# Performance work log

Measured on AMD Instinct MI355X. Metric: run time of the kernel, lower is better.

Reference implementation:

```python
import jax, jax.numpy as jnp
import numpy as np

N, E, D, ED, G = 50000, 800000, 64, 32, 50


def setup_inputs() -> dict:
    key = jax.random.key(0)
    ks = jax.random.split(key, 24)
    s = 0.05
    inp = {
        "x": jax.random.normal(ks[0], (N, D), jnp.float32),
        "edge_attr": jax.random.normal(ks[1], (E, ED), jnp.float32),
        "edge_index": jax.random.randint(ks[2], (2, E), 0, N, jnp.int64),
    }
    i = 3
    for step in range(2):
        inp[f"fe{step}_W1"] = jax.random.normal(ks[i], (2 * D + ED, D), jnp.float32) * s; i += 1
        inp[f"fe{step}_b1"] = jnp.zeros((D,), jnp.float32)
        inp[f"fe{step}_W2"] = jax.random.normal(ks[i], (D, D), jnp.float32) * s; i += 1
        inp[f"fe{step}_b2"] = jnp.zeros((D,), jnp.float32)
        inp[f"lstm{step}_Wih"] = jax.random.normal(ks[i], (D, 4 * D), jnp.float32) * s; i += 1
        inp[f"lstm{step}_Whh"] = jax.random.normal(ks[i], (D, 4 * D), jnp.float32) * s; i += 1
        inp[f"lstm{step}_bih"] = jnp.zeros((4 * D,), jnp.float32)
        inp[f"lstm{step}_bhh"] = jnp.zeros((4 * D,), jnp.float32)
    inp["gm_W"] = jax.random.normal(ks[i], (D, G), jnp.float32) * s; i += 1
    inp["gm_b"] = jnp.zeros((G,), jnp.float32)
    inp["fm_W"] = jax.random.normal(ks[i], (D, G), jnp.float32) * s; i += 1
    inp["fm_b"] = jnp.zeros((G,), jnp.float32)
    return inp


def _mpn(x, edge_attr, src, dst, W1, b1, W2, b2):
    # x_i = x[dst] (target), x_j = x[src] (source); aggregate 'add' at dst
    m = jnp.concatenate([x[dst], x[src], edge_attr], axis=1)  # [E, 2D+ED]
    m = jax.nn.relu(m @ W1 + b1) @ W2 + b2                    # [E, D]
    return jax.ops.segment_sum(m, dst, num_segments=x.shape[0])


def _lstm_cell(inp, h, c, Wih, Whh, bih, bhh):
    gates = inp @ Wih + h @ Whh + (bih + bhh)  # [N, 4D], gate order i,f,g,o
    i, f, g, o = jnp.split(gates, 4, axis=1)
    c = jax.nn.sigmoid(f) * c + jax.nn.sigmoid(i) * jnp.tanh(g)
    h = jax.nn.sigmoid(o) * jnp.tanh(c)
    return h, c


def reference(x, edge_attr, edge_index,
              fe0_W1, fe0_b1, fe0_W2, fe0_b2,
              lstm0_Wih, lstm0_Whh, lstm0_bih, lstm0_bhh,
              fe1_W1, fe1_b1, fe1_W2, fe1_b2,
              lstm1_Wih, lstm1_Whh, lstm1_bih, lstm1_bhh,
              gm_W, gm_b, fm_W, fm_b):
    src, dst = edge_index[0], edge_index[1]
    c = jnp.zeros_like(x)
    fes = [(fe0_W1, fe0_b1, fe0_W2, fe0_b2), (fe1_W1, fe1_b1, fe1_W2, fe1_b2)]
    lstms = [(lstm0_Wih, lstm0_Whh, lstm0_bih, lstm0_bhh),
             (lstm1_Wih, lstm1_Whh, lstm1_bih, lstm1_bhh)]
    for step in range(2):
        a = _mpn(x, edge_attr, src, dst, *fes[step])
        # LSTMCell(input=x, (h=a, c=c)) as in the original forward
        x, c = _lstm_cell(x, a, c, *lstms[step])
    g = jax.nn.sigmoid(x @ gm_W + gm_b)   # [N, G]
    h_v_G = x @ fm_W + fm_b               # [N, G]
    return jnp.sum(g * h_v_G, axis=0)     # [G]
```

## Files before the change

### kernel.cpp

```cpp
#include <hip/hip_runtime.h>
#include <hip/hip_bf16.h>

using short8 = __attribute__((ext_vector_type(8))) short;
using f32x4  = __attribute__((ext_vector_type(4))) float;

#define KLP 136

__device__ __forceinline__ unsigned short f2bf(float f) {
  unsigned u = __float_as_uint(f);
  u += 0x7FFFu + ((u >> 16) & 1u);
  return (unsigned short)(u >> 16);
}
__device__ __forceinline__ unsigned pack2(float a, float b) {
  return (unsigned)f2bf(a) | ((unsigned)f2bf(b) << 16);
}
#if __has_builtin(__builtin_amdgcn_rcpf)
__device__ __forceinline__ float fast_rcp(float x) { return __builtin_amdgcn_rcpf(x); }
#else
__device__ __forceinline__ float fast_rcp(float x) { return 1.f / x; }
#endif
__device__ __forceinline__ float sigm(float x) { return fast_rcp(1.f + __expf(-x)); }
__device__ __forceinline__ float tanh_f(float x) { return fmaf(2.f, sigm(2.f * x), -1.f); }

__global__ __launch_bounds__(256) void prep_simple(
    const float* __restrict__ W1_0, const float* __restrict__ Wih0,
    const float* __restrict__ bih0, const float* __restrict__ bhh0,
    const float* __restrict__ W1_1, const float* __restrict__ Wih1,
    const float* __restrict__ bih1, const float* __restrict__ bhh1,
    const float* __restrict__ gmW, const float* __restrict__ fmW,
    unsigned short* __restrict__ W1T,
    unsigned short* __restrict__ WcT,
    float* __restrict__ bG,
    unsigned short* __restrict__ WrT)
{
  int t = blockIdx.x * 256 + threadIdx.x;
  const int per = 10240 + 16384 + 256;
  if (t >= 2 * per + 8192) return;
  if (t >= 2 * per) {
    int r2 = t - 2 * per;
    int o = r2 >> 6, k = r2 & 63;
    float v = 0.f;
    if (o < 50) v = gmW[k * 50 + o];
    else if (o >= 64 && o < 114) v = fmW[k * 50 + (o - 64)];
    WrT[o * 64 + k] = f2bf(v);
    return;
  }
  int step = t / per, r = t % per;
  const float* W1  = step ? W1_1 : W1_0;
  const float* Wih = step ? Wih1 : Wih0;
  const float* bih = step ? bih1 : bih0;
  const float* bhh = step ? bhh1 : bhh0;
  if (r < 10240) {
    int o = r / 160, k = r % 160;
    W1T[step * 10240 + o * 160 + k] = f2bf(W1[k * 64 + o]);
  } else if (r < 26624) {
    int rr = r - 10240;
    int g = rr >> 6, k = rr & 63;
    WcT[step * 32768 + g * 128 + k] = f2bf(Wih[k * 256 + g]);
  } else {
    int g = r - 26624;
    bG[step * 256 + g] = bih[g] + bhh[g];
  }
}

__global__ __launch_bounds__(256) void prep_merge(
    const float* __restrict__ W2_0, const float* __restrict__ Whh0, const float* __restrict__ b2_0,
    const float* __restrict__ W2_1, const float* __restrict__ Whh1, const float* __restrict__ b2_1,
    unsigned short* __restrict__ WcT,
    float* __restrict__ b2h)
{
  int t = blockIdx.x * 256 + threadIdx.x;
  if (t < 32768) {
    int step = t >> 14, r = t & 16383;
    int g = r >> 6, k = r & 63;
    const float* W2  = step ? W2_1 : W2_0;
    const float* Whh = step ? Whh1 : Whh0;
    float v = 0.f;
    for (int j = 0; j < 64; ++j) v = fmaf(W2[k * 64 + j], Whh[j * 256 + g], v);
    WcT[step * 32768 + g * 128 + 64 + k] = f2bf(v);
  } else if (t < 33280) {
    int r = t - 32768;
    int step = r >> 8, g = r & 255;
    const float* b2  = step ? b2_1 : b2_0;
    const float* Whh = step ? Whh1 : Whh0;
    float v = 0.f;
    for (int j = 0; j < 64; ++j) v = fmaf(b2[j], Whh[j * 256 + g], v);
    b2h[step * 256 + g] = v;
  }
}

__global__ __launch_bounds__(256) void convert_x(
    const float* __restrict__ x, unsigned short* __restrict__ xb, int n)
{
  int i = blockIdx.x * 256 + threadIdx.x;
  if (i < n) xb[i] = f2bf(x[i]);
}

__global__ __launch_bounds__(256) void hist_kernel(
    const int* __restrict__ dstI, int* __restrict__ hist, int E)
{
  int e = blockIdx.x * 256 + threadIdx.x;
  if (e < E) atomicAdd(&hist[dstI[e]], 1);
}

__global__ __launch_bounds__(256) void scan_part(
    const int* __restrict__ hist, int2* __restrict__ blockTot, int N)
{
  __shared__ int sD[256], sS[256];
  int t = threadIdx.x;
  int n = blockIdx.x * 256 + t;
  int d = (n < N) ? hist[n] : 0;
  int sg = (d + 15) >> 4;
  sD[t] = d; sS[t] = sg;
  __syncthreads();
  #pragma unroll
  for (int off = 128; off; off >>= 1) {
    if (t < off) { sD[t] += sD[t + off]; sS[t] += sS[t + off]; }
    __syncthreads();
  }
  if (t == 0) blockTot[blockIdx.x] = make_int2(sD[0], sS[0]);
}

__global__ __launch_bounds__(256) void scan_mid(
    const int2* __restrict__ blockTot, int2* __restrict__ blockBase,
    int* __restrict__ nSegTot, int nb)
{
  __shared__ int sD[256], sS[256];
  int t = threadIdx.x;
  int d = 0, s = 0;
  if (t < nb) { int2 v = blockTot[t]; d = v.x; s = v.y; }
  sD[t] = d; sS[t] = s;
  __syncthreads();
  #pragma unroll
  for (int off = 1; off < 256; off <<= 1) {
    int vd = (t >= off) ? sD[t - off] : 0;
    int vs = (t >= off) ? sS[t - off] : 0;
    __syncthreads();
    sD[t] += vd; sS[t] += vs;
    __syncthreads();
  }
  if (t < nb) blockBase[t] = make_int2(sD[t] - d, sS[t] - s);
  if (t == nb - 1) *nSegTot = sS[t];
}

__global__ __launch_bounds__(256) void scan_final(
    const int* __restrict__ hist, const int2* __restrict__ blockBase,
    int* __restrict__ cursor, int4* __restrict__ segInfo, int N)
{
  __shared__ int sD[256], sS[256];
  int t = threadIdx.x;
  int n = blockIdx.x * 256 + t;
  int d = (n < N) ? hist[n] : 0;
  int sg = (d + 15) >> 4;
  sD[t] = d; sS[t] = sg;
  __syncthreads();
  #pragma unroll
  for (int off = 1; off < 256; off <<= 1) {
    int vd = (t >= off) ? sD[t - off] : 0;
    int vs = (t >= off) ? sS[t - off] : 0;
    __syncthreads();
    sD[t] += vd; sS[t] += vs;
    __syncthreads();
  }
  if (n < N) {
    int2 bb = blockBase[blockIdx.x];
    int degBase = bb.x + sD[t] - d;
    int segBase = bb.y + sS[t] - sg;
    cursor[n] = degBase;
    for (int j = 0; j < sg; ++j)
      segInfo[segBase + j] = make_int4(degBase + j * 16, n, min(d - j * 16, 16), 0);
  }
}

__global__ __launch_bounds__(256) void perm_build(
    const int* __restrict__ srcI, const int* __restrict__ dstI,
    int* __restrict__ cursor, int* __restrict__ ePerm,
    int* __restrict__ srcS, int E)
{
  int e = blockIdx.x * 256 + threadIdx.x;
  if (e >= E) return;
  int d = dstI[e];
  int p = atomicAdd(&cursor[d], 1);
  ePerm[p] = e;
  srcS[p] = srcI[e];
}

__global__ __launch_bounds__(256) void edge_gemm_reg(
    const unsigned short* __restrict__ xb,
    const float* __restrict__ ea,
    const int* __restrict__ ePerm,
    const int* __restrict__ srcS,
    const int4* __restrict__ segInfo,
    const int* __restrict__ nSegPtr,
    const unsigned short* __restrict__ W1T,
    const float* __restrict__ b1,
    float* __restrict__ aggrH)
{
  const int t = threadIdx.x;
  const int w = t >> 6, l = t & 63;
  const int quad = l >> 4, lr = l & 15;

  short8 bF[5][4];
  #pragma unroll
  for (int kc = 0; kc < 5; ++kc)
    #pragma unroll
    for (int n = 0; n < 4; ++n)
      bF[kc][n] = *(const short8*)(W1T + (n * 16 + lr) * 160 + kc * 32 + quad * 8);
  float bb[4];
  #pragma unroll
  for (int n = 0; n < 4; ++n) bb[n] = b1[n * 16 + lr];

  const int nSeg = *nSegPtr;
  const int W = gridDim.x * 4;
  int s = blockIdx.x * 4 + w;
  if (s >= nSeg) return;
  int4 si = segInfo[s];
  {
    int pos0 = si.x + min(lr, si.z - 1);
  }
  int pos = si.x + min(lr, si.z - 1);
  int src = srcS[pos];
  int ep  = ePerm[pos];

  while (true) {
    const int sn = s + W;
    const bool more = sn < nSeg;
    int4 si_n = si;
    if (more) si_n = segInfo[sn];

    const int node = si.y, cnt = si.z;

    const short8* pd = (const short8*)(xb + (long long)node * 64);
    const short8* ps = (const short8*)(xb + (long long)src * 64);
    const float4* pe = (const float4*)(ea + (long long)ep * 32 + quad * 8);
    short8 a0 = pd[quad];
    short8 a1 = pd[4 + quad];
    short8 a2 = ps[quad];
    short8 a3 = ps[4 + quad];
    float4 e0 = pe[0];
    float4 e1 = pe[1];

    int src_n = src, ep_n = ep;
    if (more) {
      int pos_n = si_n.x + min(lr, si_n.z - 1);
      src_n = srcS[pos_n];
      ep_n  = ePerm[pos_n];
    }

    union { uint4 u; short8 s8; } cv;
    cv.u = make_uint4(pack2(e0.x, e0.y), pack2(e0.z, e0.w),
                      pack2(e1.x, e1.y), pack2(e1.z, e1.w));
    short8 a4 = cv.s8;

    f32x4 acc[4] = {};
    #pragma unroll
    for (int n = 0; n < 4; ++n) acc[n] = __builtin_amdgcn_mfma_f32_16x16x32_bf16(a0, bF[0][n], acc[n], 0, 0, 0);
    #pragma unroll
    for (int n = 0; n < 4; ++n) acc[n] = __builtin_amdgcn_mfma_f32_16x16x32_bf16(a1, bF[1][n], acc[n], 0, 0, 0);
    #pragma unroll
    for (int n = 0; n < 4; ++n) acc[n] = __builtin_amdgcn_mfma_f32_16x16x32_bf16(a2, bF[2][n], acc[n], 0, 0, 0);
    #pragma unroll
    for (int n = 0; n < 4; ++n) acc[n] = __builtin_amdgcn_mfma_f32_16x16x32_bf16(a3, bF[3][n], acc[n], 0, 0, 0);
    #pragma unroll
    for (int n = 0; n < 4; ++n) acc[n] = __builtin_amdgcn_mfma_f32_16x16x32_bf16(a4, bF[4][n], acc[n], 0, 0, 0);

    #pragma unroll
    for (int n = 0; n < 4; ++n) {
      float sum = 0.f;
      #pragma unroll
      for (int rr = 0; rr < 4; ++rr) {
        float v = fmaxf(acc[n][rr] + bb[n], 0.f);
        sum += (quad * 4 + rr < cnt) ? v : 0.f;
      }
      sum += __shfl_xor(sum, 16);
      sum += __shfl_xor(sum, 32);
      if (quad == 0) unsafeAtomicAdd(&aggrH[(long long)node * 64 + n * 16 + lr], sum);
    }

    if (!more) break;
    s = sn; si = si_n; src = src_n; ep = ep_n;
  }
}

__global__ __launch_bounds__(256) void lstm3(
    const unsigned short* __restrict__ xbin,
    const float* __restrict__ aggrH,
    const float* __restrict__ cin,
    float* __restrict__ cout,
    const unsigned short* __restrict__ WcT,
    const float* __restrict__ bG,
    const float* __restrict__ b2h,
    const int* __restrict__ degA,
    unsigned short* __restrict__ xbout,
    int nNodes)
{
  __shared__ unsigned short sIn[64 * KLP];
  __shared__ unsigned short sW[64 * KLP];
  __shared__ float sBG[256], sB2h[256];
  const int t = threadIdx.x;
  sBG[t] = bG[t];
  sB2h[t] = b2h[t];

  const int base_n = blockIdx.x * 64;
  const int nl = t >> 2, q = t & 3;
  const int node = base_n + nl;
  unsigned short* rowp = sIn + nl * KLP;
  if (node < nNodes) {
    const uint4* px = (const uint4*)(xbin + (long long)node * 64);
    *(uint4*)(rowp + q * 16)     = px[q * 2];
    *(uint4*)(rowp + q * 16 + 8) = px[q * 2 + 1];
    const float4* pg = (const float4*)(aggrH + (long long)node * 64) + q * 4;
    float4 g0 = pg[0], g1 = pg[1], g2 = pg[2], g3 = pg[3];
    *(uint4*)(rowp + 64 + q * 16) =
        make_uint4(pack2(g0.x, g0.y), pack2(g0.z, g0.w), pack2(g1.x, g1.y), pack2(g1.z, g1.w));
    *(uint4*)(rowp + 64 + q * 16 + 8) =
        make_uint4(pack2(g2.x, g2.y), pack2(g2.z, g2.w), pack2(g3.x, g3.y), pack2(g3.z, g3.w));
  } else {
    *(uint4*)(rowp + q * 16)          = make_uint4(0, 0, 0, 0);
    *(uint4*)(rowp + q * 16 + 8)      = make_uint4(0, 0, 0, 0);
    *(uint4*)(rowp + 64 + q * 16)     = make_uint4(0, 0, 0, 0);
    *(uint4*)(rowp + 64 + q * 16 + 8) = make_uint4(0, 0, 0, 0);
  }

  const int w = t >> 6, l = t & 63, quad = l >> 4, lr = l & 15;
  const int row0 = w * 16;
  f32x4 acc[16] = {};
  for (int grp = 0; grp < 4; ++grp) {
    const uint4* gw = (const uint4*)WcT + (long long)(grp * 64) * 16;
    uint4* lw = (uint4*)sW;
    {
      int o0 = t >> 4, s4 = t & 15;
      #pragma unroll
      for (int pp = 0; pp < 4; ++pp) {
        int o = pp * 16 + o0;
        lw[o * 17 + s4] = gw[o * 16 + s4];
      }
    }
    __syncthreads();
    #pragma unroll
    for (int kc = 0; kc < 4; ++kc) {
      short8 aF = *(const short8*)(sIn + (row0 + lr) * KLP + kc * 32 + quad * 8);
      #pragma unroll
      for (int nt = 0; nt < 4; ++nt) {
        short8 bF = *(const short8*)(sW + (nt * 16 + lr) * KLP + kc * 32 + quad * 8);
        acc[grp * 4 + nt] = __builtin_amdgcn_mfma_f32_16x16x32_bf16(aF, bF, acc[grp * 4 + nt], 0, 0, 0);
      }
    }
    __syncthreads();
  }

  #pragma unroll
  for (int nt = 0; nt < 4; ++nt) {
    #pragma unroll
    for (int rr = 0; rr < 4; ++rr) {
      int node2 = base_n + row0 + quad * 4 + rr;
      if (node2 < nNodes) {
        int col = nt * 16 + lr;
        long long off = (long long)node2 * 64 + col;
        float dg = (float)degA[node2];
        float iv = acc[nt][rr]      + sBG[col]       + dg * sB2h[col];
        float fv = acc[4 + nt][rr]  + sBG[64 + col]  + dg * sB2h[64 + col];
        float gv = acc[8 + nt][rr]  + sBG[128 + col] + dg * sB2h[128 + col];
        float ov = acc[12 + nt][rr] + sBG[192 + col] + dg * sB2h[192 + col];
        float cOld = cin ? cin[off] : 0.f;
        float cN = sigm(fv) * cOld + sigm(iv) * tanh_f(gv);
        float hN = sigm(ov) * tanh_f(cN);
        cout[off] = cN;
        xbout[off] = f2bf(hN);
      }
    }
  }
}

__global__ __launch_bounds__(256) void readout(
    const unsigned short* __restrict__ xq,
    const unsigned short* __restrict__ WrT,
    const float* __restrict__ gb, const float* __restrict__ fb,
    float* __restrict__ out, int nNodes)
{
  __shared__ unsigned short sX[64 * 72];
  __shared__ unsigned short sW[128 * 72];
  __shared__ float sOut[4][64];
  __shared__ float sGb[64], sFb[64];
  const int t = threadIdx.x;
  {
    const uint4* gw = (const uint4*)WrT;
    uint4* lw = (uint4*)sW;
    #pragma unroll
    for (int pp = 0; pp < 4; ++pp) {
      int idx = t + pp * 256;
      int o = idx >> 3, s = idx & 7;
      lw[o * 9 + s] = gw[idx];
    }
    if (t < 50)      { sGb[t] = gb[t]; sFb[t] = fb[t]; }
    else if (t < 64) { sGb[t] = 0.f;   sFb[t] = 0.f; }
  }
  const int base = blockIdx.x * 64;
  const int nl = t >> 2, q = t & 3;
  const int node = base + nl;
  {
    uint4* dst = (uint4*)(sX + nl * 72 + q * 16);
    if (node < nNodes) {
      const uint4* px = (const uint4*)(xq + (long long)node * 64);
      dst[0] = px[q * 2];
      dst[1] = px[q * 2 + 1];
    } else {
      dst[0] = make_uint4(0, 0, 0, 0);
      dst[1] = make_uint4(0, 0, 0, 0);
    }
  }
  __syncthreads();

  const int w = t >> 6, l = t & 63, quad = l >> 4, lr = l & 15;
  f32x4 acc[8] = {};
  #pragma unroll
  for (int kc = 0; kc < 2; ++kc) {
    short8 aF = *(const short8*)(sX + (w * 16 + lr) * 72 + kc * 32 + quad * 8);
    #pragma unroll
    for (int n = 0; n < 8; ++n) {
      short8 bF = *(const short8*)(sW + (n * 16 + lr) * 72 + kc * 32 + quad * 8);
      acc[n] = __builtin_amdgcn_mfma_f32_16x16x32_bf16(aF, bF, acc[n], 0, 0, 0);
    }
  }
  #pragma unroll
  for (int n = 0; n < 4; ++n) {
    float val = 0.f;
    #pragma unroll
    for (int rr = 0; rr < 4; ++rr) {
      int nd = base + w * 16 + quad * 4 + rr;
      if (nd < nNodes) {
        int jj = n * 16 + lr;
        float gv = sigm(acc[n][rr] + sGb[jj]);
        float fv = acc[n + 4][rr] + sFb[jj];
        val += gv * fv;
      }
    }
    val += __shfl_xor(val, 16);
    val += __shfl_xor(val, 32);
    if (quad == 0) sOut[w][n * 16 + lr] = val;
  }
  __syncthreads();
  if (t < 50) {
    float s = sOut[0][t] + sOut[1][t] + sOut[2][t] + sOut[3][t];
    unsafeAtomicAdd(&out[t], s);
  }
}

extern "C" void kernel_launch(void* const* d_in, const int* in_sizes, int n_in,
                              void* d_out, int out_size, void* d_ws, size_t ws_size,
                              hipStream_t stream)
{
  const float* x      = (const float*)d_in[0];
  const float* ea     = (const float*)d_in[1];
  const int*   ei     = (const int*)d_in[2];
  const float* fe0_W1 = (const float*)d_in[3];
  const float* fe0_b1 = (const float*)d_in[4];
  const float* fe0_W2 = (const float*)d_in[5];
  const float* fe0_b2 = (const float*)d_in[6];
  const float* l0_Wih = (const float*)d_in[7];
  const float* l0_Whh = (const float*)d_in[8];
  const float* l0_bih = (const float*)d_in[9];
  const float* l0_bhh = (const float*)d_in[10];
  const float* fe1_W1 = (const float*)d_in[11];
  const float* fe1_b1 = (const float*)d_in[12];
  const float* fe1_W2 = (const float*)d_in[13];
  const float* fe1_b2 = (const float*)d_in[14];
  const float* l1_Wih = (const float*)d_in[15];
  const float* l1_Whh = (const float*)d_in[16];
  const float* l1_bih = (const float*)d_in[17];
  const float* l1_bhh = (const float*)d_in[18];
  const float* gm_W   = (const float*)d_in[19];
  const float* gm_b   = (const float*)d_in[20];
  const float* fm_W   = (const float*)d_in[21];
  const float* fm_b   = (const float*)d_in[22];

  const int N = in_sizes[0] / 64;
  const int E = in_sizes[1] / 32;
  const int* srcI = ei;
  const int* dstI = ei + E;

  char* ws = (char*)d_ws;
  unsigned short* xb0     = (unsigned short*)(ws + 0);
  unsigned short* xb1     = (unsigned short*)(ws + 6400000);
  float*          aggrH   = (float*)(ws + 12800000);
  float*          cbuf    = (float*)(ws + 25600000);
  int*            ePerm   = (int*)(ws + 38400000);
  int*            srcS    = (int*)(ws + 89601024);
  int4*           segInfo = (int4*)(ws + 92801088);
  int*            histA   = (int*)(ws + 94401280);
  int*            curA    = (int*)(ws + 94601280);
  unsigned short* W1T     = (unsigned short*)(ws + 94801280);
  unsigned short* WcT     = (unsigned short*)(ws + 94842240);
  float*          bG      = (float*)(ws + 94973312);
  float*          b2h     = (float*)(ws + 94975360);
  unsigned short* WrT     = (unsigned short*)(ws + 94977408);
  int*            nSegPtr = (int*)(ws + 94993792);
  int2*           blockTot  = (int2*)(ws + 94993856);
  int2*           blockBase = (int2*)(ws + 94995904);

  hipMemsetAsync(d_out, 0, out_size * sizeof(float), stream);
  hipMemsetAsync(histA, 0, (size_t)N * 4, stream);

  prep_simple<<<(2 * 26880 + 8192 + 255) / 256, 256, 0, stream>>>(
      fe0_W1, l0_Wih, l0_bih, l0_bhh,
      fe1_W1, l1_Wih, l1_bih, l1_bhh,
      gm_W, fm_W, W1T, WcT, bG, WrT);
  prep_merge<<<(33280 + 255) / 256, 256, 0, stream>>>(
      fe0_W2, l0_Whh, fe0_b2, fe1_W2, l1_Whh, fe1_b2, WcT, b2h);
  convert_x<<<(N * 64 + 255) / 256, 256, 0, stream>>>(x, xb0, N * 64);

  const int nb = (N + 255) / 256;
  hist_kernel<<<(E + 255) / 256, 256, 0, stream>>>(dstI, histA, E);
  scan_part<<<nb, 256, 0, stream>>>(histA, blockTot, N);
  scan_mid<<<1, 256, 0, stream>>>(blockTot, blockBase, nSegPtr, nb);
  scan_final<<<nb, 256, 0, stream>>>(histA, blockBase, curA, segInfo, N);
  perm_build<<<(E + 255) / 256, 256, 0, stream>>>(srcI, dstI, curA, ePerm, srcS, E);

  const int nodeBlocks = (N + 63) / 64;

  hipMemsetAsync(aggrH, 0, (size_t)N * 64 * 4, stream);
  edge_gemm_reg<<<2048, 256, 0, stream>>>(xb0, ea, ePerm, srcS, segInfo, nSegPtr,
                                          W1T, fe0_b1, aggrH);
  lstm3<<<nodeBlocks, 256, 0, stream>>>(xb0, aggrH, nullptr, cbuf, WcT, bG, b2h,
                                        histA, xb1, N);

  hipMemsetAsync(aggrH, 0, (size_t)N * 64 * 4, stream);
  edge_gemm_reg<<<2048, 256, 0, stream>>>(xb1, ea, ePerm, srcS, segInfo, nSegPtr,
                                          W1T + 10240, fe1_b1, aggrH);
  lstm3<<<nodeBlocks, 256, 0, stream>>>(xb1, aggrH, cbuf, cbuf, WcT + 32768,
                                        bG + 256, b2h + 256, histA, xb0, N);

  readout<<<nodeBlocks, 256, 0, stream>>>(xb0, WrT, gm_b, fm_b, (float*)d_out, N);
}
```

Measured before the change: 507.0 us.

## Pre-convert edge attributes to bf16 and stage W1 fragments in LDS

Adds a one-time kernel that converts edge_attr to bf16 so both edge GEMM passes gather half the bytes per edge and skip per-use packing. The edge GEMM also moves its W1 B-fragments from 20 short8 registers per lane into a 20 KB shared-memory stash, read on every MFMA, to cut register pressure and raise occupancy. In exchange it pays an extra full pass over edge_attr plus a bf16 workspace region, and adds LDS reads inside the inner loop. ePerm is moved to a new workspace offset to make room.

```diff
diff --git a/kernel.cpp b/kernel.cpp
--- a/kernel.cpp
+++ b/kernel.cpp
@@ -96,6 +96,17 @@
   if (i < n) xb[i] = f2bf(x[i]);
 }
 
+__global__ __launch_bounds__(256) void convert_ea(
+    const float* __restrict__ ea, unsigned short* __restrict__ eaB, int n8)
+{
+  int i = blockIdx.x * 256 + threadIdx.x;
+  if (i >= n8) return;
+  const float4* p = (const float4*)(ea + (long long)i * 8);
+  float4 a0 = p[0], a1 = p[1];
+  *(uint4*)(eaB + (long long)i * 8) =
+      make_uint4(pack2(a0.x, a0.y), pack2(a0.z, a0.w), pack2(a1.x, a1.y), pack2(a1.z, a1.w));
+}
+
 __global__ __launch_bounds__(256) void hist_kernel(
     const int* __restrict__ dstI, int* __restrict__ hist, int E)
 {
@@ -187,7 +198,7 @@
 
 __global__ __launch_bounds__(256) void edge_gemm_reg(
     const unsigned short* __restrict__ xb,
-    const float* __restrict__ ea,
+    const unsigned short* __restrict__ eaB,
     const int* __restrict__ ePerm,
     const int* __restrict__ srcS,
     const int4* __restrict__ segInfo,
@@ -196,28 +207,30 @@
     const float* __restrict__ b1,
     float* __restrict__ aggrH)
 {
+  __shared__ unsigned short stash[20 * 64 * 8];
   const int t = threadIdx.x;
   const int w = t >> 6, l = t & 63;
   const int quad = l >> 4, lr = l & 15;
 
-  short8 bF[5][4];
-  #pragma unroll
-  for (int kc = 0; kc < 5; ++kc)
-    #pragma unroll
-    for (int n = 0; n < 4; ++n)
-      bF[kc][n] = *(const short8*)(W1T + (n * 16 + lr) * 160 + kc * 32 + quad * 8);
+  #pragma unroll
+  for (int p = 0; p < 5; ++p) {
+    int idx = p * 256 + t;
+    int grp = idx >> 6, ll = idx & 63;
+    int kc = grp >> 2, n = grp & 3;
+    int row = n * 16 + (ll & 15);
+    int col = kc * 32 + (ll >> 4) * 8;
+    *(uint4*)(stash + idx * 8) = *(const uint4*)(W1T + row * 160 + col);
+  }
   float bb[4];
   #pragma unroll
   for (int n = 0; n < 4; ++n) bb[n] = b1[n * 16 + lr];
+  __syncthreads();
 
   const int nSeg = *nSegPtr;
   const int W = gridDim.x * 4;
   int s = blockIdx.x * 4 + w;
   if (s >= nSeg) return;
   int4 si = segInfo[s];
-  {
-    int pos0 = si.x + min(lr, si.z - 1);
-  }
   int pos = si.x + min(lr, si.z - 1);
   int src = srcS[pos];
   int ep  = ePerm[pos];
@@ -232,13 +245,11 @@
 
     const short8* pd = (const short8*)(xb + (long long)node * 64);
     const short8* ps = (const short8*)(xb + (long long)src * 64);
-    const float4* pe = (const float4*)(ea + (long long)ep * 32 + quad * 8);
     short8 a0 = pd[quad];
     short8 a1 = pd[4 + quad];
     short8 a2 = ps[quad];
     short8 a3 = ps[4 + quad];
-    float4 e0 = pe[0];
-    float4 e1 = pe[1];
+    short8 a4 = *(const short8*)(eaB + (long long)ep * 32 + quad * 8);
 
     int src_n = src, ep_n = ep;
     if (more) {
@@ -247,22 +258,16 @@
       ep_n  = ePerm[pos_n];
     }
 
-    union { uint4 u; short8 s8; } cv;
-    cv.u = make_uint4(pack2(e0.x, e0.y), pack2(e0.z, e0.w),
-                      pack2(e1.x, e1.y), pack2(e1.z, e1.w));
-    short8 a4 = cv.s8;
-
     f32x4 acc[4] = {};
     #pragma unroll
-    for (int n = 0; n < 4; ++n) acc[n] = __builtin_amdgcn_mfma_f32_16x16x32_bf16(a0, bF[0][n], acc[n], 0, 0, 0);
-    #pragma unroll
-    for (int n = 0; n < 4; ++n) acc[n] = __builtin_amdgcn_mfma_f32_16x16x32_bf16(a1, bF[1][n], acc[n], 0, 0, 0);
-    #pragma unroll
-    for (int n = 0; n < 4; ++n) acc[n] = __builtin_amdgcn_mfma_f32_16x16x32_bf16(a2, bF[2][n], acc[n], 0, 0, 0);
-    #pragma unroll
-    for (int n = 0; n < 4; ++n) acc[n] = __builtin_amdgcn_mfma_f32_16x16x32_bf16(a3, bF[3][n], acc[n], 0, 0, 0);
-    #pragma unroll
-    for (int n = 0; n < 4; ++n) acc[n] = __builtin_amdgcn_mfma_f32_16x16x32_bf16(a4, bF[4][n], acc[n], 0, 0, 0);
+    for (int kc = 0; kc < 5; ++kc) {
+      short8 aX = (kc == 0) ? a0 : (kc == 1) ? a1 : (kc == 2) ? a2 : (kc == 3) ? a3 : a4;
+      #pragma unroll
+      for (int n = 0; n < 4; ++n) {
+        short8 bFr = *(const short8*)(stash + (((kc << 2) | n) * 64 + l) * 8);
+        acc[n] = __builtin_amdgcn_mfma_f32_16x16x32_bf16(aX, bFr, acc[n], 0, 0, 0);
+      }
+    }
 
     #pragma unroll
     for (int n = 0; n < 4; ++n) {
@@ -484,7 +489,7 @@
   unsigned short* xb1     = (unsigned short*)(ws + 6400000);
   float*          aggrH   = (float*)(ws + 12800000);
   float*          cbuf    = (float*)(ws + 25600000);
-  int*            ePerm   = (int*)(ws + 38400000);
+  unsigned short* eaB     = (unsigned short*)(ws + 38400000);
   int*            srcS    = (int*)(ws + 89601024);
   int4*           segInfo = (int4*)(ws + 92801088);
   int*            histA   = (int*)(ws + 94401280);
@@ -497,6 +502,7 @@
   int*            nSegPtr = (int*)(ws + 94993792);
   int2*           blockTot  = (int2*)(ws + 94993856);
   int2*           blockBase = (int2*)(ws + 94995904);
+  int*            ePerm   = (int*)(ws + 95000000);
 
   hipMemsetAsync(d_out, 0, out_size * sizeof(float), stream);
   hipMemsetAsync(histA, 0, (size_t)N * 4, stream);
@@ -508,6 +514,7 @@
   prep_merge<<<(33280 + 255) / 256, 256, 0, stream>>>(
       fe0_W2, l0_Whh, fe0_b2, fe1_W2, l1_Whh, fe1_b2, WcT, b2h);
   convert_x<<<(N * 64 + 255) / 256, 256, 0, stream>>>(x, xb0, N * 64);
+  convert_ea<<<(E * 4 + 255) / 256, 256, 0, stream>>>(ea, eaB, E * 4);
 
   const int nb = (N + 255) / 256;
   hist_kernel<<<(E + 255) / 256, 256, 0, stream>>>(dstI, histA, E);
@@ -519,13 +526,13 @@
   const int nodeBlocks = (N + 63) / 64;
 
   hipMemsetAsync(aggrH, 0, (size_t)N * 64 * 4, stream);
-  edge_gemm_reg<<<2048, 256, 0, stream>>>(xb0, ea, ePerm, srcS, segInfo, nSegPtr,
+  edge_gemm_reg<<<2048, 256, 0, stream>>>(xb0, eaB, ePerm, srcS, segInfo, nSegPtr,
                                           W1T, fe0_b1, aggrH);
   lstm3<<<nodeBlocks, 256, 0, stream>>>(xb0, aggrH, nullptr, cbuf, WcT, bG, b2h,
                                         histA, xb1, N);
 
   hipMemsetAsync(aggrH, 0, (size_t)N * 64 * 4, stream);
-  edge_gemm_reg<<<2048, 256, 0, stream>>>(xb1, ea, ePerm, srcS, segInfo, nSegPtr,
+  edge_gemm_reg<<<2048, 256, 0, stream>>>(xb1, eaB, ePerm, srcS, segInfo, nSegPtr,
                                           W1T + 10240, fe1_b1, aggrH);
   lstm3<<<nodeBlocks, 256, 0, stream>>>(xb1, aggrH, cbuf, cbuf, WcT + 32768,
                                         bG + 256, b2h + 256, histA, xb0, N);
```

Measured after the change: 500.6 us. Within noise of the previous version (-1.3%).
